# Performance work log

Hardware: AMD Instinct MI355X
Metric: run time of the kernel (lower is better)

Reference implementation:

```python
import jax, jax.numpy as jnp
import numpy as np

B, S, D, E, H, K = 2, 2048, 1024, 8, 4096, 2  # batch, seq, n_embed, num_experts, 4*n_embed, top_k


def setup_inputs() -> dict:
    key = jax.random.key(0)
    ks = jax.random.split(key, 10)
    w = lambda k, shape: (jax.random.normal(k, shape, jnp.float32) * 0.02)
    return {
        "x": jax.random.normal(ks[0], (B, S, D), jnp.float32),
        "noise": jax.random.normal(ks[1], (B, S, E), jnp.float32),  # replaces torch.randn_like
        "Wr": w(ks[2], (D, E)),  # topkroute_linear
        "br": jnp.zeros((E,), jnp.float32),
        "Wn": w(ks[3], (D, E)),  # noise_linear
        "bn": jnp.zeros((E,), jnp.float32),
        "W1": w(ks[4], (E, D, H)),  # per-expert first Linear
        "b1": jnp.zeros((E, H), jnp.float32),
        "W2": w(ks[5], (E, H, D)),  # per-expert second Linear
        "b2": jnp.zeros((E, D), jnp.float32),
    }


def reference(x, noise, Wr, br, Wn, bn, W1, b1, W2, b2):
    # --- NoisyTopkRouter ---
    logits = jnp.einsum('bsd,de->bse', x, Wr) + br
    noise_logits = jnp.einsum('bsd,de->bse', x, Wn) + bn
    noisy_logits = logits + noise * jax.nn.softplus(noise_logits)
    _, topi = jax.lax.top_k(noisy_logits, K)                      # [B,S,K]
    sel = (topi[..., :, None] == jnp.arange(E)).any(axis=-2)      # [B,S,E] bool
    gates = jax.nn.softmax(jnp.where(sel, noisy_logits, -jnp.inf), axis=-1)  # sparse softmax
    softmax_gating = jax.nn.softmax(logits, axis=-1)

    # --- expert dispatch: gate is exactly 0 for non-selected experts, so the
    # masked gather/scatter loop equals a gate-weighted sum over all experts ---
    h = jax.nn.relu(jnp.einsum('bsd,edh->ebsh', x, W1) + b1[:, None, None, :])  # [E,B,S,H]
    y = jnp.einsum('ebsh,ehd->ebsd', h, W2) + b2[:, None, None, :]              # [E,B,S,D]
    final = jnp.einsum('bse,ebsd->bsd', gates, y)
    return final, softmax_gating
```

## Files before the change

kernel.cpp:

```cpp
#include <hip/hip_runtime.h>
#include <stdint.h>

#define T_TOK 4096
#define Dm    1024
#define Em    8
#define Hm    4096
#define NSLOT (2 * T_TOK)
#define KSPLIT 2

typedef __bf16 bf16x8 __attribute__((ext_vector_type(8)));
typedef float  f32x4  __attribute__((ext_vector_type(4)));

__device__ __forceinline__ unsigned short f2bf(float f) {
  union { float f; unsigned int u; } c; c.f = f;
  unsigned int u = c.u;
  unsigned int r = u + 0x7fffu + ((u >> 16) & 1u);
  return (unsigned short)(r >> 16);
}

__device__ __forceinline__ void async16(const void* g, void* l) {
  __builtin_amdgcn_global_load_lds(
      (const __attribute__((address_space(1))) void*)g,
      (__attribute__((address_space(3))) void*)l, 16, 0, 0);
}

__global__ void transpose_cvt_kernel(const float* __restrict__ src,
                                     unsigned short* __restrict__ dst,
                                     int R, int C) {
  __shared__ float tile[32][33];
  const int e = blockIdx.z;
  const float* s = src + (size_t)e * R * C;
  unsigned short* d = dst + (size_t)e * R * C;
  const int c0 = blockIdx.x * 32, r0 = blockIdx.y * 32;
  for (int i = threadIdx.y; i < 32; i += 8)
    tile[i][threadIdx.x] = s[(size_t)(r0 + i) * C + c0 + threadIdx.x];
  __syncthreads();
  for (int i = threadIdx.y; i < 32; i += 8)
    d[(size_t)(c0 + i) * R + r0 + threadIdx.x] = f2bf(tile[threadIdx.x][i]);
}

__global__ void cvt_x_kernel(const float* __restrict__ x, unsigned short* __restrict__ xbf) {
  const int i = blockIdx.x * 256 + threadIdx.x;
  float4 v = ((const float4*)x)[i];
  ushort4 o;
  o.x = f2bf(v.x); o.y = f2bf(v.y); o.z = f2bf(v.z); o.w = f2bf(v.w);
  ((ushort4*)xbf)[i] = o;
}

__global__ __launch_bounds__(256) void router_kernel(
    const float* __restrict__ x, const float* __restrict__ noise,
    const float* __restrict__ Wr, const float* __restrict__ br,
    const float* __restrict__ Wn, const float* __restrict__ bn,
    float* __restrict__ out_gating, int* __restrict__ lists,
    int* __restrict__ counts, int* __restrict__ expt,
    int* __restrict__ pos, float* __restrict__ gsel) {
  const int wave = threadIdx.x >> 6, lane = threadIdx.x & 63;
  const int t = blockIdx.x * 4 + wave;
  const float* xt = x + (size_t)t * Dm;
  float accR[Em] = {}, accN[Em] = {};
  for (int d = lane; d < Dm; d += 64) {
    const float xv = xt[d];
    const float* wr = Wr + d * Em;
    const float* wn = Wn + d * Em;
#pragma unroll
    for (int e = 0; e < Em; e++) { accR[e] += xv * wr[e]; accN[e] += xv * wn[e]; }
  }
#pragma unroll
  for (int e = 0; e < Em; e++)
    for (int off = 32; off > 0; off >>= 1) {
      accR[e] += __shfl_down(accR[e], off, 64);
      accN[e] += __shfl_down(accN[e], off, 64);
    }
  if (lane == 0) {
    float lg[Em], ny[Em];
#pragma unroll
    for (int e = 0; e < Em; e++) {
      lg[e] = accR[e] + br[e];
      float nl = accN[e] + bn[e];
      float sp = fmaxf(nl, 0.f) + log1pf(expf(-fabsf(nl)));
      ny[e] = lg[e] + noise[(size_t)t * Em + e] * sp;
    }
    int i0 = 0;
#pragma unroll
    for (int e = 1; e < Em; e++) if (ny[e] > ny[i0]) i0 = e;
    int i1 = (i0 == 0) ? 1 : 0;
#pragma unroll
    for (int e = 0; e < Em; e++) if (e != i0 && ny[e] > ny[i1]) i1 = e;
    const float e1 = expf(ny[i1] - ny[i0]);
    const float g0 = 1.f / (1.f + e1), g1 = e1 / (1.f + e1);
    float m = lg[0];
#pragma unroll
    for (int e = 1; e < Em; e++) m = fmaxf(m, lg[e]);
    float s = 0.f;
#pragma unroll
    for (int e = 0; e < Em; e++) s += expf(lg[e] - m);
#pragma unroll
    for (int e = 0; e < Em; e++) out_gating[(size_t)t * Em + e] = expf(lg[e] - m) / s;
    int p0 = atomicAdd(&counts[i0], 1); lists[i0 * T_TOK + p0] = t;
    int p1 = atomicAdd(&counts[i1], 1); lists[i1 * T_TOK + p1] = t;
    expt[2 * t] = i0; expt[2 * t + 1] = i1;
    pos[2 * t] = p0;  pos[2 * t + 1] = p1;
    gsel[2 * t] = g0; gsel[2 * t + 1] = g1;
  }
}

__global__ __launch_bounds__(256) void gemm1_kernel(
    const unsigned short* __restrict__ xbf, const unsigned short* __restrict__ w1bf,
    const float* __restrict__ b1, const int* __restrict__ counts,
    const int* __restrict__ lists, unsigned short* __restrict__ hbuf) {
  const int e = blockIdx.z;
  const int cnt = counts[e];
  const int m0 = blockIdx.x * 128;
  if (m0 >= cnt) return;
  const int n0 = blockIdx.y * 128;
  int base = 0;
  for (int i = 0; i < e; i++) base += counts[i];

  __shared__ __align__(16) unsigned short As[2][128 * 32];
  __shared__ __align__(16) unsigned short Bs[2][128 * 32];
  __shared__ int tok[128];

  const int tid = threadIdx.x;
  if (tid < 128) {
    int m = m0 + tid;
    tok[tid] = (m < cnt) ? lists[e * T_TOK + m] : 0;
  }
  __syncthreads();

  const int part = tid & 3;
  const int r0 = tid >> 2;
  const int r1 = r0 + 64;
  const size_t gA0 = (size_t)tok[r0] * Dm + part * 8;
  const size_t gA1 = (size_t)tok[r1] * Dm + part * 8;
  const size_t gB0 = ((size_t)e * Hm + n0 + r0) * Dm + part * 8;
  const size_t gB1 = ((size_t)e * Hm + n0 + r1) * Dm + part * 8;

  const int lane = tid & 63, wv = tid >> 6;
  const int quad = lane >> 4, l15 = lane & 15;
  const int wm = (wv >> 1) * 64, wn = (wv & 1) * 64;
  const int lds_off = wv * 512;

  f32x4 acc[4][4] = {};

  async16(xbf + gA0, As[0] + lds_off);
  async16(xbf + gA1, As[0] + 2048 + lds_off);
  async16(w1bf + gB0, Bs[0] + lds_off);
  async16(w1bf + gB1, Bs[0] + 2048 + lds_off);

  const int NI = Dm / 32;
  for (int it = 0; it < NI; it++) {
    const int cur = it & 1;
    __syncthreads();
    if (it + 1 < NI) {
      const int k0 = (it + 1) * 32;
      const int nb = cur ^ 1;
      async16(xbf + gA0 + k0, As[nb] + lds_off);
      async16(xbf + gA1 + k0, As[nb] + 2048 + lds_off);
      async16(w1bf + gB0 + k0, Bs[nb] + lds_off);
      async16(w1bf + gB1 + k0, Bs[nb] + 2048 + lds_off);
    }
    bf16x8 af[4], bfv[4];
#pragma unroll
    for (int i = 0; i < 4; i++)
      af[i] = *(const bf16x8*)(As[cur] + (wm + i * 16 + l15) * 32 + quad * 8);
#pragma unroll
    for (int j = 0; j < 4; j++)
      bfv[j] = *(const bf16x8*)(Bs[cur] + (wn + j * 16 + l15) * 32 + quad * 8);
#pragma unroll
    for (int i = 0; i < 4; i++)
#pragma unroll
      for (int j = 0; j < 4; j++)
        acc[i][j] = __builtin_amdgcn_mfma_f32_16x16x32_bf16(af[i], bfv[j], acc[i][j], 0, 0, 0);
  }

#pragma unroll
  for (int i = 0; i < 4; i++)
#pragma unroll
    for (int r = 0; r < 4; r++) {
      const int ml = wm + i * 16 + quad * 4 + r;
      const int m = m0 + ml;
      if (m < cnt) {
#pragma unroll
        for (int j = 0; j < 4; j++) {
          const int n = n0 + wn + j * 16 + l15;
          float v = acc[i][j][r] + b1[(size_t)e * Hm + n];
          v = fmaxf(v, 0.f);
          hbuf[(size_t)(base + m) * Hm + n] = f2bf(v);
        }
      }
    }
}

__global__ __launch_bounds__(256) void gemm2_kernel(
    const unsigned short* __restrict__ hbuf, const unsigned short* __restrict__ w2bf,
    const int* __restrict__ counts, float* __restrict__ ybuf) {
  const int e = blockIdx.z >> 1;
  const int ks = blockIdx.z & 1;
  const int cnt = counts[e];
  const int m0 = blockIdx.x * 128;
  if (m0 >= cnt) return;
  const int n0 = blockIdx.y * 128;
  int base = 0;
  for (int i = 0; i < e; i++) base += counts[i];
  const int kbase = ks * (Hm / KSPLIT);

  __shared__ __align__(16) unsigned short As[2][128 * 32];
  __shared__ __align__(16) unsigned short Bs[2][128 * 32];

  const int tid = threadIdx.x;
  const int part = tid & 3;
  const int r0 = tid >> 2;
  const int r1 = r0 + 64;
  const int rowA0 = min(base + m0 + r0, NSLOT - 1);
  const int rowA1 = min(base + m0 + r1, NSLOT - 1);
  const size_t gA0 = (size_t)rowA0 * Hm + kbase + part * 8;
  const size_t gA1 = (size_t)rowA1 * Hm + kbase + part * 8;
  const size_t gB0 = ((size_t)e * Dm + n0 + r0) * Hm + kbase + part * 8;
  const size_t gB1 = ((size_t)e * Dm + n0 + r1) * Hm + kbase + part * 8;

  const int lane = tid & 63, wv = tid >> 6;
  const int quad = lane >> 4, l15 = lane & 15;
  const int wm = (wv >> 1) * 64, wn = (wv & 1) * 64;
  const int lds_off = wv * 512;

  f32x4 acc[4][4] = {};

  async16(hbuf + gA0, As[0] + lds_off);
  async16(hbuf + gA1, As[0] + 2048 + lds_off);
  async16(w2bf + gB0, Bs[0] + lds_off);
  async16(w2bf + gB1, Bs[0] + 2048 + lds_off);

  const int NI = Hm / KSPLIT / 32;
  for (int it = 0; it < NI; it++) {
    const int cur = it & 1;
    __syncthreads();
    if (it + 1 < NI) {
      const int k0 = (it + 1) * 32;
      const int nb = cur ^ 1;
      async16(hbuf + gA0 + k0, As[nb] + lds_off);
      async16(hbuf + gA1 + k0, As[nb] + 2048 + lds_off);
      async16(w2bf + gB0 + k0, Bs[nb] + lds_off);
      async16(w2bf + gB1 + k0, Bs[nb] + 2048 + lds_off);
    }
    bf16x8 af[4], bfv[4];
#pragma unroll
    for (int i = 0; i < 4; i++)
      af[i] = *(const bf16x8*)(As[cur] + (wm + i * 16 + l15) * 32 + quad * 8);
#pragma unroll
    for (int j = 0; j < 4; j++)
      bfv[j] = *(const bf16x8*)(Bs[cur] + (wn + j * 16 + l15) * 32 + quad * 8);
#pragma unroll
    for (int i = 0; i < 4; i++)
#pragma unroll
      for (int j = 0; j < 4; j++)
        acc[i][j] = __builtin_amdgcn_mfma_f32_16x16x32_bf16(af[i], bfv[j], acc[i][j], 0, 0, 0);
  }

  float* yb = ybuf + (size_t)ks * NSLOT * Dm;
#pragma unroll
  for (int i = 0; i < 4; i++)
#pragma unroll
    for (int r = 0; r < 4; r++) {
      const int ml = wm + i * 16 + quad * 4 + r;
      const int m = m0 + ml;
      if (m < cnt) {
#pragma unroll
        for (int j = 0; j < 4; j++) {
          const int n = n0 + wn + j * 16 + l15;
          yb[(size_t)(base + m) * Dm + n] = acc[i][j][r];
        }
      }
    }
}

__global__ __launch_bounds__(256) void combine_kernel(
    const float* __restrict__ ybuf, const float* __restrict__ b2,
    const int* __restrict__ counts, const int* __restrict__ expt,
    const int* __restrict__ pos, const float* __restrict__ gsel,
    float* __restrict__ out) {
  const int t = blockIdx.x;
  const int e0 = expt[2 * t], e1 = expt[2 * t + 1];
  const float g0 = gsel[2 * t], g1 = gsel[2 * t + 1];
  int b0 = 0, b1 = 0;
  for (int i = 0; i < e0; i++) b0 += counts[i];
  for (int i = 0; i < e1; i++) b1 += counts[i];
  const size_t s0 = (size_t)(b0 + pos[2 * t]) * Dm;
  const size_t s1 = (size_t)(b1 + pos[2 * t + 1]) * Dm;
  const size_t half = (size_t)NSLOT * Dm;
  const int c = threadIdx.x * 4;
  float4 y0a = *(const float4*)(ybuf + s0 + c);
  float4 y0b = *(const float4*)(ybuf + half + s0 + c);
  float4 y1a = *(const float4*)(ybuf + s1 + c);
  float4 y1b = *(const float4*)(ybuf + half + s1 + c);
  float4 z0 = *(const float4*)(b2 + (size_t)e0 * Dm + c);
  float4 z1 = *(const float4*)(b2 + (size_t)e1 * Dm + c);
  float4 o;
  o.x = g0 * (y0a.x + y0b.x + z0.x) + g1 * (y1a.x + y1b.x + z1.x);
  o.y = g0 * (y0a.y + y0b.y + z0.y) + g1 * (y1a.y + y1b.y + z1.y);
  o.z = g0 * (y0a.z + y0b.z + z0.z) + g1 * (y1a.z + y1b.z + z1.z);
  o.w = g0 * (y0a.w + y0b.w + z0.w) + g1 * (y1a.w + y1b.w + z1.w);
  *(float4*)(out + (size_t)t * Dm + c) = o;
}

extern "C" void kernel_launch(void* const* d_in, const int* in_sizes, int n_in,
                              void* d_out, int out_size, void* d_ws, size_t ws_size,
                              hipStream_t stream) {
  const float* x     = (const float*)d_in[0];
  const float* noise = (const float*)d_in[1];
  const float* Wr    = (const float*)d_in[2];
  const float* br    = (const float*)d_in[3];
  const float* Wn    = (const float*)d_in[4];
  const float* bn    = (const float*)d_in[5];
  const float* W1    = (const float*)d_in[6];
  const float* b1    = (const float*)d_in[7];
  const float* W2    = (const float*)d_in[8];
  const float* b2    = (const float*)d_in[9];

  float* out        = (float*)d_out;
  float* out_gating = out + (size_t)T_TOK * Dm;

  char* ws = (char*)d_ws;
  unsigned short* w1bf = (unsigned short*)(ws);
  unsigned short* w2bf = (unsigned short*)(ws + 67108864);
  unsigned short* xbf  = (unsigned short*)(ws + 134217728);
  unsigned short* hbuf = (unsigned short*)(ws + 142606336);
  float* ybuf          = (float*)(ws);
  int*   lists         = (int*)(ws + 209715200);
  int*   expt          = (int*)(ws + 209846272);
  int*   pos           = (int*)(ws + 209879040);
  float* gsel          = (float*)(ws + 209911808);
  int*   counts        = (int*)(ws + 209944576);

  hipMemsetAsync(counts, 0, Em * sizeof(int), stream);

  transpose_cvt_kernel<<<dim3(Hm / 32, Dm / 32, Em), dim3(32, 8), 0, stream>>>(W1, w1bf, Dm, Hm);
  transpose_cvt_kernel<<<dim3(Dm / 32, Hm / 32, Em), dim3(32, 8), 0, stream>>>(W2, w2bf, Hm, Dm);
  cvt_x_kernel<<<(T_TOK * Dm / 4) / 256, 256, 0, stream>>>(x, xbf);

  router_kernel<<<T_TOK / 4, 256, 0, stream>>>(x, noise, Wr, br, Wn, bn,
                                               out_gating, lists, counts, expt, pos, gsel);

  gemm1_kernel<<<dim3(16, Hm / 128, Em), 256, 0, stream>>>(xbf, w1bf, b1, counts, lists, hbuf);
  gemm2_kernel<<<dim3(16, Dm / 128, Em * KSPLIT), 256, 0, stream>>>(hbuf, w2bf, counts, ybuf);
  combine_kernel<<<T_TOK, 256, 0, stream>>>(ybuf, b2, counts, expt, pos, gsel, out);
}
```

Measured before the change: 876.4 us.

## Triple-buffer LDS tiles in expert GEMMs with explicit vmcnt waits

Both expert GEMM kernels go from double to triple buffering of the A and B tiles in LDS, with loads issued two k-steps ahead. The implicit sync is replaced by an explicit s_waitcnt vmcnt(4) plus s_barrier, so the most recent stage's loads can stay in flight during compute. This aims to hide more global-load latency per k-iteration. In exchange LDS use grows by half, which may lower occupancy, and correctness depends on the hand-tuned vmcnt count matching the number of outstanding loads.

```diff
diff --git a/kernel.cpp b/kernel.cpp
--- a/kernel.cpp
+++ b/kernel.cpp
@@ -116,8 +116,8 @@
   int base = 0;
   for (int i = 0; i < e; i++) base += counts[i];
 
-  __shared__ __align__(16) unsigned short As[2][128 * 32];
-  __shared__ __align__(16) unsigned short Bs[2][128 * 32];
+  __shared__ __align__(16) unsigned short As[3][128 * 32];
+  __shared__ __align__(16) unsigned short Bs[3][128 * 32];
   __shared__ int tok[128];
 
   const int tid = threadIdx.x;
@@ -142,18 +142,28 @@
 
   f32x4 acc[4][4] = {};
 
-  async16(xbf + gA0, As[0] + lds_off);
-  async16(xbf + gA1, As[0] + 2048 + lds_off);
-  async16(w1bf + gB0, Bs[0] + lds_off);
-  async16(w1bf + gB1, Bs[0] + 2048 + lds_off);
+  async16(xbf + gA0,       As[0] + lds_off);
+  async16(xbf + gA1,       As[0] + 2048 + lds_off);
+  async16(w1bf + gB0,      Bs[0] + lds_off);
+  async16(w1bf + gB1,      Bs[0] + 2048 + lds_off);
+  async16(xbf + gA0 + 32,  As[1] + lds_off);
+  async16(xbf + gA1 + 32,  As[1] + 2048 + lds_off);
+  async16(w1bf + gB0 + 32, Bs[1] + lds_off);
+  async16(w1bf + gB1 + 32, Bs[1] + 2048 + lds_off);
 
   const int NI = Dm / 32;
-  for (int it = 0; it < NI; it++) {
-    const int cur = it & 1;
-    __syncthreads();
-    if (it + 1 < NI) {
-      const int k0 = (it + 1) * 32;
-      const int nb = cur ^ 1;
+  int cur = 0;
+  for (int it = 0; it < NI; ++it) {
+    if (it < NI - 1) {
+      asm volatile("s_waitcnt vmcnt(4)" ::: "memory");
+    } else {
+      asm volatile("s_waitcnt vmcnt(0)" ::: "memory");
+    }
+    __builtin_amdgcn_s_barrier();
+    __builtin_amdgcn_sched_barrier(0);
+    if (it + 2 < NI) {
+      const int k0 = (it + 2) * 32;
+      int nb = cur + 2; if (nb >= 3) nb -= 3;
       async16(xbf + gA0 + k0, As[nb] + lds_off);
       async16(xbf + gA1 + k0, As[nb] + 2048 + lds_off);
       async16(w1bf + gB0 + k0, Bs[nb] + lds_off);
@@ -171,6 +181,7 @@
 #pragma unroll
       for (int j = 0; j < 4; j++)
         acc[i][j] = __builtin_amdgcn_mfma_f32_16x16x32_bf16(af[i], bfv[j], acc[i][j], 0, 0, 0);
+    cur = (cur == 2) ? 0 : cur + 1;
   }
 
 #pragma unroll
@@ -204,8 +215,8 @@
   for (int i = 0; i < e; i++) base += counts[i];
   const int kbase = ks * (Hm / KSPLIT);
 
-  __shared__ __align__(16) unsigned short As[2][128 * 32];
-  __shared__ __align__(16) unsigned short Bs[2][128 * 32];
+  __shared__ __align__(16) unsigned short As[3][128 * 32];
+  __shared__ __align__(16) unsigned short Bs[3][128 * 32];
 
   const int tid = threadIdx.x;
   const int part = tid & 3;
@@ -225,18 +236,28 @@
 
   f32x4 acc[4][4] = {};
 
-  async16(hbuf + gA0, As[0] + lds_off);
-  async16(hbuf + gA1, As[0] + 2048 + lds_off);
-  async16(w2bf + gB0, Bs[0] + lds_off);
-  async16(w2bf + gB1, Bs[0] + 2048 + lds_off);
+  async16(hbuf + gA0,       As[0] + lds_off);
+  async16(hbuf + gA1,       As[0] + 2048 + lds_off);
+  async16(w2bf + gB0,       Bs[0] + lds_off);
+  async16(w2bf + gB1,       Bs[0] + 2048 + lds_off);
+  async16(hbuf + gA0 + 32,  As[1] + lds_off);
+  async16(hbuf + gA1 + 32,  As[1] + 2048 + lds_off);
+  async16(w2bf + gB0 + 32,  Bs[1] + lds_off);
+  async16(w2bf + gB1 + 32,  Bs[1] + 2048 + lds_off);
 
   const int NI = Hm / KSPLIT / 32;
-  for (int it = 0; it < NI; it++) {
-    const int cur = it & 1;
-    __syncthreads();
-    if (it + 1 < NI) {
-      const int k0 = (it + 1) * 32;
-      const int nb = cur ^ 1;
+  int cur = 0;
+  for (int it = 0; it < NI; ++it) {
+    if (it < NI - 1) {
+      asm volatile("s_waitcnt vmcnt(4)" ::: "memory");
+    } else {
+      asm volatile("s_waitcnt vmcnt(0)" ::: "memory");
+    }
+    __builtin_amdgcn_s_barrier();
+    __builtin_amdgcn_sched_barrier(0);
+    if (it + 2 < NI) {
+      const int k0 = (it + 2) * 32;
+      int nb = cur + 2; if (nb >= 3) nb -= 3;
       async16(hbuf + gA0 + k0, As[nb] + lds_off);
       async16(hbuf + gA1 + k0, As[nb] + 2048 + lds_off);
       async16(w2bf + gB0 + k0, Bs[nb] + lds_off);
@@ -254,6 +275,7 @@
 #pragma unroll
       for (int j = 0; j < 4; j++)
         acc[i][j] = __builtin_amdgcn_mfma_f32_16x16x32_bf16(af[i], bfv[j], acc[i][j], 0, 0, 0);
+    cur = (cur == 2) ? 0 : cur + 1;
   }
 
   float* yb = ybuf + (size_t)ks * NSLOT * Dm;
```

Measured after the change: 844.8 us. 1.04x faster.
